# Performance work log

Measured on AMD Instinct MI355X. Metric: run time of the kernel, lower is better.

The kernel has to match this reference:

```python
import jax, jax.numpy as jnp
import numpy as np

NUM_HEADS = 16
ROPE_BASE = 10000.0


def _rope_tables(head_dim, seq_len, dtype=jnp.float32):
    # Half-split convention: rotate first half against second half.
    inv_freq = 1.0 / (ROPE_BASE ** (jnp.arange(0, head_dim, 2, dtype=dtype) / head_dim))
    pos = jnp.arange(seq_len, dtype=dtype)
    angles_half = jnp.einsum('s,d->sd', pos, inv_freq)          # (S, D/2)
    angles = jnp.concatenate([angles_half, angles_half], -1)     # (S, D)
    return jnp.cos(angles), jnp.sin(angles)


def _apply_rope(x, cos, sin):
    # x: (H, S, D); cos/sin: (S, D) broadcast over heads
    half = x.shape[-1] // 2
    x1, x2 = x[..., :half], x[..., half:]
    x_rot = jnp.concatenate([-x2, x1], axis=-1)
    return x * cos + x_rot * sin


def setup_inputs() -> dict:
    key = jax.random.key(0)
    S, E = 2048, 2048
    ks = jax.random.split(key, 9)
    sc = 0.02
    return {
        'x': jax.random.normal(ks[0], (S, E), jnp.float32),
        'Wq': jax.random.normal(ks[1], (E, E), jnp.float32) * sc,
        'bq': jax.random.normal(ks[2], (E,), jnp.float32) * sc,
        'Wk': jax.random.normal(ks[3], (E, E), jnp.float32) * sc,
        'bk': jax.random.normal(ks[4], (E,), jnp.float32) * sc,
        'Wv': jax.random.normal(ks[5], (E, E), jnp.float32) * sc,
        'bv': jax.random.normal(ks[6], (E,), jnp.float32) * sc,
        'Wo': jax.random.normal(ks[7], (E, E), jnp.float32) * sc,
        'bo': jax.random.normal(ks[8], (E,), jnp.float32) * sc,
    }


def reference(x, Wq, bq, Wk, bk, Wv, bv, Wo, bo):
    S, E = x.shape
    H = NUM_HEADS
    D = E // H
    scale = D ** 0.5
    cos, sin = _rope_tables(D, S, x.dtype)

    def proj(W, b):
        return (x @ W.T + b).reshape(S, H, D).transpose(1, 0, 2)  # (H, S, D)

    q = _apply_rope(proj(Wq, bq), cos, sin)
    k = _apply_rope(proj(Wk, bk), cos, sin)
    v = proj(Wv, bv)

    scores = jnp.einsum('hsd,htd->hst', q, k) / scale  # (H, S, S)
    attn = jax.nn.softmax(scores, axis=-1)
    out = jnp.einsum('hst,htd->hsd', attn, v)          # (H, S, D)
    # Faithful to the original's transpose(0,1).view(S,E) on a (1,H,S,D)
    # tensor: an in-order (head-major) flatten reinterpreted as (S, E).
    out = out.reshape(S, E)
    return out @ Wo.T + bo
```

## Files before the change

### kernel.cpp

```cpp
#include <hip/hip_runtime.h>

#define SDIM 2048
#define EDIM 2048
#define NHEAD 16
#define DHEAD 128

typedef __attribute__((ext_vector_type(8))) short short8;
typedef __attribute__((ext_vector_type(4))) float floatx4;

__device__ __forceinline__ float bf2f(ushort u) {
    union { uint i; float f; } v; v.i = ((uint)u) << 16; return v.f;
}
__device__ __forceinline__ ushort f2bf(float f) {
    union { float f; uint i; } v; v.f = f;
    uint r = v.i + 0x7fff + ((v.i >> 16) & 1);
    return (ushort)(r >> 16);
}

__device__ __forceinline__ void gload_lds16(const ushort* g, ushort* l) {
    __builtin_amdgcn_global_load_lds(
        (const __attribute__((address_space(1))) void*)g,
        (__attribute__((address_space(3))) void*)l, 16, 0, 0);
}

__global__ void convert5_kernel(
    const float* __restrict__ s0, const float* __restrict__ s1,
    const float* __restrict__ s2, const float* __restrict__ s3,
    const float* __restrict__ s4,
    ushort* __restrict__ d0, ushort* __restrict__ d1,
    ushort* __restrict__ d2, ushort* __restrict__ d3,
    ushort* __restrict__ d4)
{
    const float* src; ushort* dst;
    switch (blockIdx.y) {
        case 0: src = s0; dst = d0; break;
        case 1: src = s1; dst = d1; break;
        case 2: src = s2; dst = d2; break;
        case 3: src = s3; dst = d3; break;
        default: src = s4; dst = d4; break;
    }
    int i = blockIdx.x * blockDim.x + threadIdx.x;
    float4 f = ((const float4*)src)[i];
    ushort4 o;
    o.x = f2bf(f.x); o.y = f2bf(f.y); o.z = f2bf(f.z); o.w = f2bf(f.w);
    ((ushort4*)dst)[i] = o;
}

#define QPRESCALE 0.12754245f

template <typename OUTT, int KSPLIT, int VT_WHICH, bool ROPE>
__global__ __launch_bounds__(256) void gemm_bt(
    const ushort* __restrict__ A,
    const ushort* __restrict__ B0, const ushort* __restrict__ B1, const ushort* __restrict__ B2,
    const float* __restrict__ s0, const float* __restrict__ s1, const float* __restrict__ s2,
    OUTT* __restrict__ C0, OUTT* __restrict__ C1, OUTT* __restrict__ C2,
    int nbpm)
{
    __shared__ __align__(16) ushort smem[2 * 128 * 32];
    ushort* a_s = smem;
    ushort* b_s = smem + 128 * 32;

    const int tid = threadIdx.x;
    const int wave = tid >> 6, lane = tid & 63;
    const int l15 = lane & 15, quad = lane >> 4;
    const int wm = wave & 1, wn = wave >> 1;
    const int bm = blockIdx.x * 128;
    const int which = blockIdx.y / nbpm;
    const int n0 = (blockIdx.y % nbpm) * 128;

    const ushort* B;
    const float*  bia;
    OUTT*         C;
    const ushort* Abase;
    if constexpr (KSPLIT == 2) {
        B = B0; bia = s0; C = C0;
        Abase = A + which * (EDIM / 2);
    } else {
        B   = (which == 0) ? B0 : (which == 1) ? B1 : B2;
        bia = (which == 0) ? s0 : (which == 1) ? s1 : s2;
        C   = (which == 0) ? C0 : (which == 1) ? C1 : C2;
        Abase = A;
    }
    const ushort* Bbase = (KSPLIT == 2) ? B + which * (EDIM / 2) : B;

    floatx4 acc[4][4];
#pragma unroll
    for (int i = 0; i < 4; i++)
#pragma unroll
        for (int j = 0; j < 4; j++) acc[i][j] = (floatx4)0.0f;

    const int t1 = tid + 256;
    const int row0 = tid >> 2, kc0 = (tid & 3) * 8;
    const int row1 = t1 >> 2,  kc1 = (t1 & 3) * 8;

    for (int k0 = 0; k0 < EDIM / KSPLIT; k0 += 32) {
        __syncthreads();
        gload_lds16(Abase + (size_t)(bm + row0) * EDIM + k0 + kc0, a_s + tid * 8);
        gload_lds16(Abase + (size_t)(bm + row1) * EDIM + k0 + kc1, a_s + t1 * 8);
        gload_lds16(Bbase + (size_t)(n0 + row0) * EDIM + k0 + kc0, b_s + tid * 8);
        gload_lds16(Bbase + (size_t)(n0 + row1) * EDIM + k0 + kc1, b_s + t1 * 8);
        __syncthreads();

        short8 af[4], bf[4];
#pragma unroll
        for (int mt = 0; mt < 4; mt++)
            af[mt] = *(const short8*)(a_s + (wm * 64 + mt * 16 + l15) * 32 + quad * 8);
#pragma unroll
        for (int nt = 0; nt < 4; nt++)
            bf[nt] = *(const short8*)(b_s + (wn * 64 + nt * 16 + l15) * 32 + quad * 8);
#pragma unroll
        for (int mt = 0; mt < 4; mt++)
#pragma unroll
            for (int nt = 0; nt < 4; nt++)
                acc[mt][nt] = __builtin_amdgcn_mfma_f32_16x16x32_bf16(af[mt], bf[nt], acc[mt][nt], 0, 0, 0);
    }

    if constexpr (KSPLIT == 2) {
#pragma unroll
        for (int nt = 0; nt < 4; nt++) {
            int col = n0 + wn * 64 + nt * 16 + l15;
            float bv = (which == 0) ? bia[col] : 0.0f;
#pragma unroll
            for (int mt = 0; mt < 4; mt++) {
#pragma unroll
                for (int r = 0; r < 4; r++) {
                    int row = bm + wm * 64 + mt * 16 + quad * 4 + r;
                    atomicAdd(&((float*)C)[(size_t)row * EDIM + col], acc[mt][nt][r] + bv);
                }
            }
        }
    } else if (VT_WHICH >= 0 && which == VT_WHICH) {
        ushort* Cv = (ushort*)C;
#pragma unroll
        for (int nt = 0; nt < 4; nt++) {
            int col = n0 + wn * 64 + nt * 16 + l15;
            int h = col >> 7, d = col & 127;
            float bv = bia[col];
#pragma unroll
            for (int mt = 0; mt < 4; mt++) {
                int s = bm + wm * 64 + mt * 16 + quad * 4;
                ushort4 pk;
                pk.x = f2bf(acc[mt][nt][0] + bv);
                pk.y = f2bf(acc[mt][nt][1] + bv);
                pk.z = f2bf(acc[mt][nt][2] + bv);
                pk.w = f2bf(acc[mt][nt][3] + bv);
                *(ushort4*)(Cv + (size_t)h * SDIM * DHEAD + (size_t)d * SDIM + s) = pk;
            }
        }
    } else if constexpr (ROPE) {
        float* xch = (float*)smem;
        float bv[4], invf[4];
#pragma unroll
        for (int nt = 0; nt < 4; nt++) {
            bv[nt]   = bia[n0 + wn * 64 + nt * 16 + l15];
            invf[nt] = __expf((float)(nt * 16 + l15) * -0.14391157f);
        }
        const float psc = (which == 0) ? QPRESCALE : 1.0f;
        const int mybase = wave * 1024 + quad * 16 + l15;
        const int pbase  = (wave ^ 2) * 1024 + quad * 16 + l15;
#pragma unroll
        for (int mt = 0; mt < 4; mt++) {
            __syncthreads();
#pragma unroll
            for (int nt = 0; nt < 4; nt++)
#pragma unroll
                for (int r = 0; r < 4; r++)
                    xch[mybase + nt * 256 + r * 64] = acc[mt][nt][r] + bv[nt];
            __syncthreads();
#pragma unroll
            for (int nt = 0; nt < 4; nt++) {
                int col = n0 + wn * 64 + nt * 16 + l15;
#pragma unroll
                for (int r = 0; r < 4; r++) {
                    int row = bm + wm * 64 + mt * 16 + quad * 4 + r;
                    float v = acc[mt][nt][r] + bv[nt];
                    float w = xch[pbase + nt * 256 + r * 64];
                    float ang = (float)row * invf[nt];
                    float rev = ang * 0.15915494309f;
                    rev -= floorf(rev);
                    float ar = rev * 6.28318530718f;
                    float sn = __sinf(ar), cs = __cosf(ar);
                    float o = (wn == 0) ? (v * cs - w * sn) : (v * cs + w * sn);
                    ((ushort*)C)[(size_t)row * EDIM + col] = f2bf(o * psc);
                }
            }
        }
    } else {
#pragma unroll
        for (int nt = 0; nt < 4; nt++) {
            int col = n0 + wn * 64 + nt * 16 + l15;
            float bv = bia[col];
#pragma unroll
            for (int mt = 0; mt < 4; mt++) {
#pragma unroll
                for (int r = 0; r < 4; r++) {
                    int row = bm + wm * 64 + mt * 16 + quad * 4 + r;
                    float v = acc[mt][nt][r] + bv;
                    if constexpr (sizeof(OUTT) == 2)
                        ((ushort*)C)[(size_t)row * EDIM + col] = f2bf(v);
                    else
                        ((float*)C)[(size_t)row * EDIM + col] = v;
                }
            }
        }
    }
}

#define MFIX2 17.31234049f
__global__ __launch_bounds__(256, 4) void attn_kernel(
    const ushort* __restrict__ Q, const ushort* __restrict__ K,
    const ushort* __restrict__ Vtg,
    ushort* __restrict__ Opart, float* __restrict__ Lsum,
    ushort* __restrict__ Ab, int nsplit)
{
    __shared__ __align__(16) ushort Ks[64 * 128];
    __shared__ __align__(16) ushort Vt[128 * 64];
    __shared__ __align__(16) ushort Ps[64 * 64];

    const int bid = blockIdx.x;
    const int head = bid & 15, qt = (bid >> 4) & 31, half = bid >> 9;
    const int tid = threadIdx.x, wave = tid >> 6, lane = tid & 63;
    const int l15 = lane & 15, quad = lane >> 4;
    const int l7 = l15 & 7;
    const int kstart = half * (SDIM / nsplit);
    const int ntile = (SDIM / nsplit) / 64;

    short8 qf[4];
    {
        int s = qt * 64 + wave * 16 + l15;
        const ushort* qp = Q + (size_t)s * EDIM + head * DHEAD;
#pragma unroll
        for (int kc = 0; kc < 4; kc++) qf[kc] = *(const short8*)(qp + kc * 32 + quad * 8);
    }

    floatx4 o[8];
#pragma unroll
    for (int i = 0; i < 8; i++) o[i] = (floatx4)0.0f;
    float lsum = 0.0f;

    const int krow = tid >> 4, kc8 = tid & 15;
    const int vd = tid >> 3, vc8 = tid & 7;
    const int prow = wave * 16 + l15;

    for (int kv = 0; kv < ntile; kv++) {
        const int k0 = kstart + kv * 64;
        __syncthreads();
#pragma unroll
        for (int i = 0; i < 4; i++) {
            int row = krow + i * 16;
            uint4 v = *(const uint4*)(K + (size_t)(k0 + row) * EDIM + head * DHEAD + kc8 * 8);
            *(uint4*)(Ks + row * 128 + ((kc8 ^ (row & 7)) << 3)) = v;
        }
#pragma unroll
        for (int i = 0; i < 4; i++) {
            int d = vd + i * 32;
            uint4 v = *(const uint4*)(Vtg + (size_t)head * SDIM * DHEAD + (size_t)d * SDIM + k0 + vc8 * 8);
            *(uint4*)(Vt + d * 64 + ((vc8 ^ (d & 7)) << 3)) = v;
        }
        __syncthreads();

#pragma unroll
        for (int nt = 0; nt < 4; nt++) {
            floatx4 st = (floatx4)0.0f;
#pragma unroll
            for (int kc = 0; kc < 4; kc++) {
                short8 kfr = *(const short8*)(Ks + (nt * 16 + l15) * 128 + (((kc * 4 + quad) ^ l7) << 3));
                st = __builtin_amdgcn_mfma_f32_16x16x32_bf16(kfr, qf[kc], st, 0, 0, 0);
            }
            ushort4 pk;
            float p0 = __builtin_amdgcn_exp2f(st[0] - MFIX2);
            float p1 = __builtin_amdgcn_exp2f(st[1] - MFIX2);
            float p2 = __builtin_amdgcn_exp2f(st[2] - MFIX2);
            float p3 = __builtin_amdgcn_exp2f(st[3] - MFIX2);
            lsum += (p0 + p1) + (p2 + p3);
            pk.x = f2bf(p0); pk.y = f2bf(p1); pk.z = f2bf(p2); pk.w = f2bf(p3);
            int c2 = (nt * 2 + (quad >> 1)) ^ l7;
            *(ushort4*)(Ps + prow * 64 + (c2 << 3) + ((quad & 1) << 2)) = pk;
        }

#pragma unroll
        for (int kc2 = 0; kc2 < 2; kc2++) {
            short8 af = *(const short8*)(Ps + prow * 64 + (((kc2 * 4 + quad) ^ l7) << 3));
#pragma unroll
            for (int nt2 = 0; nt2 < 8; nt2++) {
                short8 bfr = *(const short8*)(Vt + (nt2 * 16 + l15) * 64 + (((kc2 * 4 + quad) ^ l7) << 3));
                o[nt2] = __builtin_amdgcn_mfma_f32_16x16x32_bf16(af, bfr, o[nt2], 0, 0, 0);
            }
        }
    }

    lsum += __shfl_xor(lsum, 16);
    lsum += __shfl_xor(lsum, 32);

    if (nsplit == 1) {
        float invl[4];
#pragma unroll
        for (int r = 0; r < 4; r++) invl[r] = 1.0f / __shfl(lsum, quad * 4 + r, 16);
#pragma unroll
        for (int nt2 = 0; nt2 < 8; nt2++) {
#pragma unroll
            for (int r = 0; r < 4; r++) {
                int s = qt * 64 + wave * 16 + quad * 4 + r;
                int d = nt2 * 16 + l15;
                Ab[(size_t)head * SDIM * DHEAD + (size_t)s * DHEAD + d] = f2bf(o[nt2][r] * invl[r]);
            }
        }
    } else {
        size_t pb = ((size_t)half * NHEAD + head) * SDIM * DHEAD;
#pragma unroll
        for (int nt2 = 0; nt2 < 8; nt2++) {
#pragma unroll
            for (int r = 0; r < 4; r++) {
                int s = qt * 64 + wave * 16 + quad * 4 + r;
                int d = nt2 * 16 + l15;
                Opart[pb + (size_t)s * DHEAD + d] = f2bf(o[nt2][r]);
            }
        }
        if (lane < 16)
            Lsum[((size_t)half * NHEAD + head) * SDIM + qt * 64 + wave * 16 + lane] = lsum;
    }
}

__global__ void merge_kernel(const ushort* __restrict__ Opart,
                             const float* __restrict__ Lsum,
                             ushort* __restrict__ Ab)
{
    const int HS = NHEAD * SDIM;
    int t = blockIdx.x * blockDim.x + threadIdx.x;
    int row = t >> 4, c8 = (t & 15) * 8;
    float inv = 1.0f / (Lsum[row] + Lsum[HS + row] + Lsum[2 * HS + row] + Lsum[3 * HS + row]);
    float acc[8] = {0, 0, 0, 0, 0, 0, 0, 0};
#pragma unroll
    for (int p = 0; p < 4; p++) {
        union { uint4 v; ushort u[8]; } a;
        a.v = *(const uint4*)(Opart + (size_t)p * HS * DHEAD + (size_t)row * DHEAD + c8);
#pragma unroll
        for (int j = 0; j < 8; j++) acc[j] += bf2f(a.u[j]);
    }
    union { uint4 v; ushort u[8]; } ro;
#pragma unroll
    for (int j = 0; j < 8; j++) ro.u[j] = f2bf(acc[j] * inv);
    *(uint4*)(Ab + (size_t)row * DHEAD + c8) = ro.v;
}

extern "C" void kernel_launch(void* const* d_in, const int* in_sizes, int n_in,
                              void* d_out, int out_size, void* d_ws, size_t ws_size,
                              hipStream_t stream) {
    (void)in_sizes; (void)n_in; (void)out_size;
    const float* x  = (const float*)d_in[0];
    const float* Wq = (const float*)d_in[1];
    const float* bq = (const float*)d_in[2];
    const float* Wk = (const float*)d_in[3];
    const float* bk = (const float*)d_in[4];
    const float* Wv = (const float*)d_in[5];
    const float* bv = (const float*)d_in[6];
    const float* Wo = (const float*)d_in[7];
    const float* bo = (const float*)d_in[8];
    float* out = (float*)d_out;

    char* ws = (char*)d_ws;
    const size_t SEG = (size_t)EDIM * EDIM * 2;
    ushort* xb  = (ushort*)(ws + 0 * SEG);
    ushort* Wqb = (ushort*)(ws + 1 * SEG);
    ushort* Wkb = (ushort*)(ws + 2 * SEG);
    ushort* Wvb = (ushort*)(ws + 3 * SEG);
    ushort* Wob = (ushort*)(ws + 4 * SEG);
    ushort* Qb  = (ushort*)(ws + 5 * SEG);
    ushort* Kb  = (ushort*)(ws + 6 * SEG);
    ushort* Vtg = (ushort*)(ws + 7 * SEG);
    ushort* Ab  = (ushort*)(ws + 8 * SEG);
    ushort* Op  = (ushort*)(ws + 0 * SEG);
    float*  Ls  = (float*)(ws + 11 * SEG);

    const int split = (ws_size >= ((size_t)89 << 20)) ? 1 : 0;

    convert5_kernel<<<dim3(4096, 5), 256, 0, stream>>>(
        x, Wq, Wk, Wv, Wo, xb, Wqb, Wkb, Wvb, Wob);

    gemm_bt<ushort, 1, 2, true><<<dim3(16, 48), 256, 0, stream>>>(
        xb, Wqb, Wkb, Wvb, bq, bk, bv, Qb, Kb, Vtg, 16);

    if (split) {
        attn_kernel<<<2048, 256, 0, stream>>>(Qb, Kb, Vtg, Op, Ls, Ab, 4);
        merge_kernel<<<2048, 256, 0, stream>>>(Op, Ls, Ab);
        hipMemsetAsync(out, 0, (size_t)EDIM * EDIM * 4, stream);
        gemm_bt<float, 2, -1, false><<<dim3(16, 32), 256, 0, stream>>>(
            Ab, Wob, Wob, Wob, bo, bo, bo, out, out, out, 16);
    } else {
        attn_kernel<<<512, 256, 0, stream>>>(Qb, Kb, Vtg, Op, Ls, Ab, 1);
        gemm_bt<float, 1, -1, false><<<dim3(16, 16), 256, 0, stream>>>(
            Ab, Wob, Wob, Wob, bo, bo, bo, out, out, out, 16);
    }
}
```

Measured before the change: 321.9 us.

## Replace QKV projection with 256x256-tile, 8-wave pipelined GEMM kernel

Adds a dedicated QKV projection kernel that uses 256x256 output tiles with 512 threads, 64-wide K tiles and double-buffered LDS filled by direct global-to-LDS loads. The loads are swizzled and the main loop is split into four MFMA phases, each fenced by barriers and raised wave priority, so the next tile's loads overlap compute. The RoPE and V-transpose epilogues move into this kernel, and the old generic template loses those paths. Larger tiles cut redundant operand traffic, but the grid shrinks to 192 blocks and register pressure goes up.

Result: faster. 298.1 us (-7.4%).

```diff
diff --git a/kernel.cpp b/kernel.cpp
--- a/kernel.cpp
+++ b/kernel.cpp
@@ -48,6 +48,201 @@
 
 #define QPRESCALE 0.12754245f
 
+__global__ __launch_bounds__(512, 2) void gemm256_qkv(
+    const ushort* __restrict__ A,
+    const ushort* __restrict__ B0, const ushort* __restrict__ B1, const ushort* __restrict__ B2,
+    const float* __restrict__ s0, const float* __restrict__ s1, const float* __restrict__ s2,
+    ushort* __restrict__ C0, ushort* __restrict__ C1, ushort* __restrict__ Vtg)
+{
+    __shared__ __align__(16) ushort smem[2][2][2][128 * 64];
+
+    const int tid  = threadIdx.x;
+    const int lane = tid & 63;
+    const int wave = tid >> 6;
+    const int l15 = lane & 15, quad = lane >> 4, l7 = lane & 7;
+    const int wm = wave & 1, wn = wave >> 1;
+    const int bm = blockIdx.x * 256;
+    const int which = blockIdx.y >> 3;
+    const int n0 = (blockIdx.y & 7) * 256;
+
+    const ushort* Bsel = (which == 0) ? B0 : (which == 1) ? B1 : B2;
+    const float*  bia  = (which == 0) ? s0 : (which == 1) ? s1 : s2;
+
+    const int srow = tid >> 3;
+    const int sgc  = (((tid & 7) ^ ((tid >> 3) & 7)) << 3);
+
+    floatx4 acc[8][4];
+#pragma unroll
+    for (int i = 0; i < 8; i++)
+#pragma unroll
+        for (int j = 0; j < 4; j++) acc[i][j] = (floatx4)0.0f;
+
+    auto stageA = [&](int tile, int h) {
+        const ushort* g = A + (size_t)(bm + h * 128 + srow) * EDIM + tile * 64 + sgc;
+        ushort* l = &smem[tile & 1][0][h][0] + tid * 8;
+        gload_lds16(g, l);
+        gload_lds16(g + (size_t)64 * EDIM, l + 4096);
+    };
+    auto stageB = [&](int tile, int h) {
+        const ushort* g = Bsel + (size_t)(n0 + h * 128 + srow) * EDIM + tile * 64 + sgc;
+        ushort* l = &smem[tile & 1][1][h][0] + tid * 8;
+        gload_lds16(g, l);
+        gload_lds16(g + (size_t)64 * EDIM, l + 4096);
+    };
+
+    stageA(0, 0); stageA(0, 1); stageB(0, 0); stageB(0, 1);
+    stageB(1, 0); stageB(1, 1);
+    asm volatile("s_waitcnt vmcnt(4)" ::: "memory");
+    __builtin_amdgcn_s_barrier();
+
+    const int c0 = ((quad ^ l7) << 3);
+    const int c1 = (((quad + 4) ^ l7) << 3);
+    const int brow0 = (wn & 1) * 64;
+
+    short8 af[4][2], bq0[2][2], bq1[2][2];
+
+#define MFMA8(AOFF, NOFF, BQ) \
+    _Pragma("unroll") \
+    for (int kk = 0; kk < 2; kk++) \
+        _Pragma("unroll") \
+        for (int mf = 0; mf < 4; mf++) \
+            _Pragma("unroll") \
+            for (int nf = 0; nf < 2; nf++) \
+                acc[(AOFF) + mf][(NOFF) + nf] = __builtin_amdgcn_mfma_f32_16x16x32_bf16( \
+                    af[mf][kk], BQ[nf][kk], acc[(AOFF) + mf][(NOFF) + nf], 0, 0, 0);
+
+#define PH_PRE() do { \
+    asm volatile("" ::: "memory"); \
+    __builtin_amdgcn_s_barrier(); \
+    asm volatile("s_waitcnt lgkmcnt(0)" ::: "memory"); \
+    __builtin_amdgcn_sched_barrier(0); \
+    __builtin_amdgcn_s_setprio(1); \
+} while (0)
+#define PH_POST() do { \
+    __builtin_amdgcn_s_setprio(0); \
+    asm volatile("" ::: "memory"); \
+    __builtin_amdgcn_s_barrier(); \
+} while (0)
+
+    const int NTILES = EDIM / 64;
+    for (int t = 0; t < NTILES; ++t) {
+        const ushort* aH = &smem[t & 1][0][wm][0];
+        const ushort* bH = &smem[t & 1][1][wn >> 1][0];
+
+#pragma unroll
+        for (int mf = 0; mf < 4; mf++) {
+            const ushort* p = aH + (mf * 16 + l15) * 64;
+            af[mf][0] = *(const short8*)(p + c0);
+            af[mf][1] = *(const short8*)(p + c1);
+        }
+#pragma unroll
+        for (int nf = 0; nf < 2; nf++) {
+            const ushort* p = bH + (brow0 + nf * 16 + l15) * 64;
+            bq0[nf][0] = *(const short8*)(p + c0);
+            bq0[nf][1] = *(const short8*)(p + c1);
+        }
+        if (t + 1 < NTILES) stageA(t + 1, 0);
+        PH_PRE();
+        MFMA8(0, 0, bq0);
+        PH_POST();
+
+#pragma unroll
+        for (int nf = 0; nf < 2; nf++) {
+            const ushort* p = bH + (brow0 + 32 + nf * 16 + l15) * 64;
+            bq1[nf][0] = *(const short8*)(p + c0);
+            bq1[nf][1] = *(const short8*)(p + c1);
+        }
+        if (t + 1 < NTILES) stageA(t + 1, 1);
+        PH_PRE();
+        MFMA8(0, 2, bq1);
+        PH_POST();
+
+#pragma unroll
+        for (int mf = 0; mf < 4; mf++) {
+            const ushort* p = aH + (64 + mf * 16 + l15) * 64;
+            af[mf][0] = *(const short8*)(p + c0);
+            af[mf][1] = *(const short8*)(p + c1);
+        }
+        if (t + 2 < NTILES) stageB(t + 2, 0);
+        PH_PRE();
+        MFMA8(4, 2, bq1);
+        PH_POST();
+
+        if (t + 2 < NTILES) stageB(t + 2, 1);
+        asm volatile("" ::: "memory");
+        __builtin_amdgcn_s_barrier();
+        __builtin_amdgcn_s_setprio(1);
+        MFMA8(4, 0, bq0);
+        __builtin_amdgcn_s_setprio(0);
+        if (t < NTILES - 2) asm volatile("s_waitcnt vmcnt(4)" ::: "memory");
+        else                asm volatile("s_waitcnt vmcnt(0)" ::: "memory");
+        __builtin_amdgcn_s_barrier();
+    }
+#undef MFMA8
+#undef PH_PRE
+#undef PH_POST
+
+    if (which == 2) {
+#pragma unroll
+        for (int an = 0; an < 4; an++) {
+            int col = n0 + wn * 64 + an * 16 + l15;
+            int h = col >> 7, d = col & 127;
+            float bv = bia[col];
+            ushort* cp = Vtg + (size_t)h * SDIM * DHEAD + (size_t)d * SDIM;
+#pragma unroll
+            for (int am = 0; am < 8; am++) {
+                int s = bm + wm * 128 + am * 16 + quad * 4;
+                ushort4 pk;
+                pk.x = f2bf(acc[am][an][0] + bv);
+                pk.y = f2bf(acc[am][an][1] + bv);
+                pk.z = f2bf(acc[am][an][2] + bv);
+                pk.w = f2bf(acc[am][an][3] + bv);
+                *(ushort4*)(cp + s) = pk;
+            }
+        }
+    } else {
+        ushort* C = (which == 0) ? C0 : C1;
+        const float psc = (which == 0) ? QPRESCALE : 1.0f;
+        float* xch = (float*)smem;
+        float bv[4], invf[4];
+#pragma unroll
+        for (int an = 0; an < 4; an++) {
+            bv[an]   = bia[n0 + wn * 64 + an * 16 + l15];
+            invf[an] = __expf((float)(an * 16 + l15) * -0.14391157f);
+        }
+        const int mybase = wave * 1024 + quad * 16 + l15;
+        const int pbase  = (wave ^ 2) * 1024 + quad * 16 + l15;
+        const int rowb = bm + wm * 128 + quad * 4;
+#pragma unroll
+        for (int am = 0; am < 8; am++) {
+            __syncthreads();
+#pragma unroll
+            for (int an = 0; an < 4; an++)
+#pragma unroll
+                for (int r = 0; r < 4; r++)
+                    xch[mybase + an * 256 + r * 64] = acc[am][an][r] + bv[an];
+            __syncthreads();
+#pragma unroll
+            for (int an = 0; an < 4; an++) {
+                int col = n0 + wn * 64 + an * 16 + l15;
+#pragma unroll
+                for (int r = 0; r < 4; r++) {
+                    int row = rowb + am * 16 + r;
+                    float v = acc[am][an][r] + bv[an];
+                    float w = xch[pbase + an * 256 + r * 64];
+                    float ang = (float)row * invf[an];
+                    float rev = ang * 0.15915494309f;
+                    rev -= floorf(rev);
+                    float arad = rev * 6.28318530718f;
+                    float sn = __sinf(arad), cs = __cosf(arad);
+                    float o = ((wn & 1) == 0) ? (v * cs - w * sn) : (v * cs + w * sn);
+                    C[(size_t)row * EDIM + col] = f2bf(o * psc);
+                }
+            }
+        }
+    }
+}
+
 template <typename OUTT, int KSPLIT, int VT_WHICH, bool ROPE>
 __global__ __launch_bounds__(256) void gemm_bt(
     const ushort* __restrict__ A,
@@ -126,62 +321,6 @@
                 for (int r = 0; r < 4; r++) {
                     int row = bm + wm * 64 + mt * 16 + quad * 4 + r;
                     atomicAdd(&((float*)C)[(size_t)row * EDIM + col], acc[mt][nt][r] + bv);
-                }
-            }
-        }
-    } else if (VT_WHICH >= 0 && which == VT_WHICH) {
-        ushort* Cv = (ushort*)C;
-#pragma unroll
-        for (int nt = 0; nt < 4; nt++) {
-            int col = n0 + wn * 64 + nt * 16 + l15;
-            int h = col >> 7, d = col & 127;
-            float bv = bia[col];
-#pragma unroll
-            for (int mt = 0; mt < 4; mt++) {
-                int s = bm + wm * 64 + mt * 16 + quad * 4;
-                ushort4 pk;
-                pk.x = f2bf(acc[mt][nt][0] + bv);
-                pk.y = f2bf(acc[mt][nt][1] + bv);
-                pk.z = f2bf(acc[mt][nt][2] + bv);
-                pk.w = f2bf(acc[mt][nt][3] + bv);
-                *(ushort4*)(Cv + (size_t)h * SDIM * DHEAD + (size_t)d * SDIM + s) = pk;
-            }
-        }
-    } else if constexpr (ROPE) {
-        float* xch = (float*)smem;
-        float bv[4], invf[4];
-#pragma unroll
-        for (int nt = 0; nt < 4; nt++) {
-            bv[nt]   = bia[n0 + wn * 64 + nt * 16 + l15];
-            invf[nt] = __expf((float)(nt * 16 + l15) * -0.14391157f);
-        }
-        const float psc = (which == 0) ? QPRESCALE : 1.0f;
-        const int mybase = wave * 1024 + quad * 16 + l15;
-        const int pbase  = (wave ^ 2) * 1024 + quad * 16 + l15;
-#pragma unroll
-        for (int mt = 0; mt < 4; mt++) {
-            __syncthreads();
-#pragma unroll
-            for (int nt = 0; nt < 4; nt++)
-#pragma unroll
-                for (int r = 0; r < 4; r++)
-                    xch[mybase + nt * 256 + r * 64] = acc[mt][nt][r] + bv[nt];
-            __syncthreads();
-#pragma unroll
-            for (int nt = 0; nt < 4; nt++) {
-                int col = n0 + wn * 64 + nt * 16 + l15;
-#pragma unroll
-                for (int r = 0; r < 4; r++) {
-                    int row = bm + wm * 64 + mt * 16 + quad * 4 + r;
-                    float v = acc[mt][nt][r] + bv[nt];
-                    float w = xch[pbase + nt * 256 + r * 64];
-                    float ang = (float)row * invf[nt];
-                    float rev = ang * 0.15915494309f;
-                    rev -= floorf(rev);
-                    float ar = rev * 6.28318530718f;
-                    float sn = __sinf(ar), cs = __cosf(ar);
-                    float o = (wn == 0) ? (v * cs - w * sn) : (v * cs + w * sn);
-                    ((ushort*)C)[(size_t)row * EDIM + col] = f2bf(o * psc);
                 }
             }
         }
@@ -377,8 +516,8 @@
     convert5_kernel<<<dim3(4096, 5), 256, 0, stream>>>(
         x, Wq, Wk, Wv, Wo, xb, Wqb, Wkb, Wvb, Wob);
 
-    gemm_bt<ushort, 1, 2, true><<<dim3(16, 48), 256, 0, stream>>>(
-        xb, Wqb, Wkb, Wvb, bq, bk, bv, Qb, Kb, Vtg, 16);
+    gemm256_qkv<<<dim3(8, 24), 512, 0, stream>>>(
+        xb, Wqb, Wkb, Wvb, bq, bk, bv, Qb, Kb, Vtg);
 
     if (split) {
         attn_kernel<<<2048, 256, 0, stream>>>(Qb, Kb, Vtg, Op, Ls, Ab, 4);
```
